# Optimization experiments

Hardware: AMD Instinct MI355X
Metric: run time of the kernel (lower is better)

The kernel has to match this reference:

```python
import jax, jax.numpy as jnp
import numpy as np

ENC_IN = 512
D_MODEL = 1024
EMB_DIM = 32
IN_DIM = D_MODEL + EMB_DIM  # 1056
BATCH = 64


def setup_inputs() -> dict:
    key = jax.random.key(0)
    ks = jax.random.split(key, 12)
    s = 0.02
    return {
        "x": jax.random.normal(ks[0], (BATCH, ENC_IN, D_MODEL), dtype=jnp.float32),
        "emb": jax.random.normal(ks[1], (ENC_IN, EMB_DIM), dtype=jnp.float32) * s,
        # weights stored [in, out] (transposed vs torch Linear, same math)
        "w1": jax.random.normal(ks[2], (IN_DIM, IN_DIM), dtype=jnp.float32) * s,
        "b1": jnp.zeros((IN_DIM,), dtype=jnp.float32),
        "wq": jax.random.normal(ks[3], (IN_DIM, IN_DIM), dtype=jnp.float32) * s,
        "bq": jnp.zeros((IN_DIM,), dtype=jnp.float32),
        "wk": jax.random.normal(ks[4], (IN_DIM, IN_DIM), dtype=jnp.float32) * s,
        "bk": jnp.zeros((IN_DIM,), dtype=jnp.float32),
        "wv": jax.random.normal(ks[5], (IN_DIM, IN_DIM), dtype=jnp.float32) * s,
        "bv": jnp.zeros((IN_DIM,), dtype=jnp.float32),
        "w2": jax.random.normal(ks[6], (IN_DIM, D_MODEL), dtype=jnp.float32) * s,
        "b2": jnp.zeros((D_MODEL,), dtype=jnp.float32),
    }


def reference(x, emb, w1, b1, wq, bq, wk, bk, wv, bv, w2, b2):
    B = x.shape[0]
    # variable embedding: same for every batch element -> broadcast concat
    e = jnp.broadcast_to(emb[None, :, :], (B, ENC_IN, EMB_DIM))
    h = jnp.concatenate([x, e], axis=2)                      # [B, S, IN_DIM]
    h = jax.nn.leaky_relu(h @ w1 + b1, negative_slope=0.2)   # l1
    # hand-rolled self-attention: no scaling, softmax over last dim
    q = h @ wq + bq
    k = h @ wk + bk
    v = h @ wv + bv
    energy = jnp.einsum("bsd,btd->bst", q, k)                # [B, S, S]
    attn = jax.nn.softmax(energy, axis=-1)
    out = jnp.einsum("bst,btd->bsd", attn, v)                # [B, S, IN_DIM]
    return out @ w2 + b2                                     # [B, S, D_MODEL]
```

## Files before the change

### kernel.cpp

```cpp
#include <hip/hip_runtime.h>
#include <hip/hip_bf16.h>
#include <cstdint>

typedef __hip_bfloat16 bf16;
typedef __attribute__((ext_vector_type(8))) short short8;
typedef __attribute__((ext_vector_type(4))) float f32x4;

__device__ __forceinline__ void gload16(const bf16* g, bf16* l) {
    __builtin_amdgcn_global_load_lds(
        (__attribute__((address_space(1))) void*)g,
        (__attribute__((address_space(3))) void*)l, 16, 0, 0);
}
#define VMC(n) asm volatile("s_waitcnt vmcnt(" #n ")" ::: "memory")
__device__ __forceinline__ void bar() {
    asm volatile("" ::: "memory");
    __builtin_amdgcn_s_barrier();
    asm volatile("" ::: "memory");
}

__device__ __forceinline__ void stage_half(const bf16* __restrict__ G, int ld,
                                           int row0, int k0, bf16* lregion,
                                           int w, int lrow, int lslot)
{
    const bf16* s0 = G + (long long)(row0 + w * 8 + lrow) * ld + (k0 + lslot * 8);
    gload16(s0, lregion + (w * 64) * 8);
    gload16(s0 + (long long)64 * ld, lregion + (512 + w * 64) * 8);
}

#define LOAD_AI(dst, i_, mh, P) do { \
    _Pragma("unroll") for (int ks_ = 0; ks_ < 2; ++ks_) \
      dst[i_][ks_] = *(const short8*)((P) + ((mh) * 64 + (i_) * 16 + l15) * 64 \
                                         + (((ks_ * 4 + lq) ^ l7) * 8)); } while (0)
#define LOAD_B(nh, dst) do { _Pragma("unroll") for (int j_ = 0; j_ < 2; ++j_) { \
    _Pragma("unroll") for (int ks_ = 0; ks_ < 2; ++ks_) \
      dst[j_][ks_] = *(const short8*)(pb + (bhr + (nh) * 32 + j_ * 16 + l15) * 64 \
                                         + (((ks_ * 4 + lq) ^ l7) * 8)); } } while (0)
#define DO_Q(mh, nh, AF, BF) do { \
    __builtin_amdgcn_s_setprio(1); \
    _Pragma("unroll") for (int i_ = 0; i_ < 4; ++i_) \
      _Pragma("unroll") for (int j_ = 0; j_ < 2; ++j_) \
        _Pragma("unroll") for (int ks_ = 0; ks_ < 2; ++ks_) \
          acc[mh][nh][i_][j_] = __builtin_amdgcn_mfma_f32_16x16x32_bf16( \
              AF[i_][ks_], BF[j_][ks_], acc[mh][nh][i_][j_], 0, 0, 0); \
    __builtin_amdgcn_s_setprio(0); \
} while (0)

template<int OUT_BF16, int ACT, int HAS_BIAS, int ROUTE>
__global__ __launch_bounds__(512, 2)
void gemm256(const bf16* __restrict__ Abase, const bf16* __restrict__ Bbase,
             void* __restrict__ Cbase, const float* __restrict__ bias,
             int K, int lda, int ldb, int ldc, int nwrite,
             long long sA, long long sB, long long sC, long long segStride)
{
    __shared__ bf16 lds[2][2][2][8192];

    const int gx = gridDim.x, gy = gridDim.y;
    const int nwg = gx * gy * gridDim.z;
    const int lin = blockIdx.x + gx * (blockIdx.y + gy * blockIdx.z);
    const int qch = nwg >> 3, rch = nwg & 7;
    const int xcd = lin & 7, pos = lin >> 3;
    const int nl = (xcd < rch ? xcd * (qch + 1)
                              : rch * (qch + 1) + (xcd - rch) * qch) + pos;
    const int bz = nl / (gx * gy);
    const int rem = nl - bz * (gx * gy);
    const int by = rem / gx;
    const int bx = rem - by * gx;

    const int tid = threadIdx.x;
    const int wid = tid >> 6, lane = tid & 63;
    const int wm = wid >> 2, wn = wid & 3;
    const int l15 = lane & 15, l7 = lane & 7, lq = lane >> 4;
    const int lrow = lane >> 3, lslot = l7 ^ lrow;
    const int bhr = (wn & 1) * 64;

    const bf16* A = Abase + (long long)bz * sA;
    const bf16* B = Bbase + (long long)bz * sB;
    const int brow = by * 256, bcol = bx * 256;

    f32x4 acc[2][2][4][2] = {};
    short8 aFe[4][2], aFo[4][2], bF0[2][2], bF1[2][2];

    const int nt = K >> 6;

    stage_half(B, ldb, bcol,       0,  &lds[0][1][0][0], wid, lrow, lslot);
    stage_half(B, ldb, bcol + 128, 0,  &lds[0][1][1][0], wid, lrow, lslot);
    stage_half(A, lda, brow,       0,  &lds[0][0][0][0], wid, lrow, lslot);
    stage_half(A, lda, brow + 128, 0,  &lds[0][0][1][0], wid, lrow, lslot);
    stage_half(B, ldb, bcol,       64, &lds[1][1][0][0], wid, lrow, lslot);
    stage_half(B, ldb, bcol + 128, 64, &lds[1][1][1][0], wid, lrow, lslot);
    VMC(4);
    bar();

    for (int t = 0; t < nt; ++t) {
        const int b = t & 1;
        const bf16* pa = &lds[b][0][wm][0];
        const bf16* pb = &lds[b][1][wn >> 1][0];
        bf16* oA = &lds[b ^ 1][0][0][0];
        bf16* cB = &lds[b][1][0][0];
        const int t1 = (t + 1 == nt) ? 0 : t + 1;
        const int t2 = (t + 2 >= nt) ? t + 2 - nt : t + 2;
        const int k1 = t1 << 6, k2 = t2 << 6;

        LOAD_B(0, bF0);
        LOAD_AI(aFe, 0, 0, pa); LOAD_AI(aFe, 1, 0, pa);
        LOAD_AI(aFe, 2, 0, pa); LOAD_AI(aFe, 3, 0, pa);
        LOAD_B(1, bF1);
        stage_half(A, lda, brow, k1, oA, wid, lrow, lslot);
        bar();
        DO_Q(0, 0, aFe, bF0);
        bar();

        LOAD_AI(aFo, 0, 1, pa); LOAD_AI(aFo, 1, 1, pa);
        stage_half(A, lda, brow + 128, k1, oA + 8192, wid, lrow, lslot);
        bar();
        DO_Q(0, 1, aFe, bF1);
        bar();

        LOAD_AI(aFo, 2, 1, pa); LOAD_AI(aFo, 3, 1, pa);
        stage_half(B, ldb, bcol, k2, cB, wid, lrow, lslot);
        bar();
        DO_Q(1, 1, aFo, bF1);
        bar();

        stage_half(B, ldb, bcol + 128, k2, cB + 8192, wid, lrow, lslot);
        bar();
        DO_Q(1, 0, aFo, bF0);
        VMC(4);
        bar();
    }
    VMC(0);

    const long long cofs0 = (long long)bz * sC;
    #pragma unroll
    for (int mh = 0; mh < 2; ++mh)
      #pragma unroll
      for (int nh = 0; nh < 2; ++nh)
        #pragma unroll
        for (int i = 0; i < 4; ++i)
          #pragma unroll
          for (int j = 0; j < 2; ++j) {
              const int gc = bcol + wn * 64 + nh * 32 + j * 16 + l15;
              int lc = gc;
              long long cofs = cofs0;
              if (ROUTE) {
                  const unsigned seg = (unsigned)gc / 1152u;
                  lc = gc - (int)(seg * 1152u);
                  cofs += (long long)seg * segStride;
              }
              const bool wr = gc < nwrite;
              const float bvv = (HAS_BIAS && wr) ? bias[gc] : 0.0f;
              const int row0 = brow + wm * 128 + mh * 64 + i * 16 + lq * 4;
              if (wr) {
                  #pragma unroll
                  for (int rr = 0; rr < 4; ++rr) {
                      float vv = acc[mh][nh][i][j][rr] + bvv;
                      if (ACT) vv = vv > 0.0f ? vv : 0.2f * vv;
                      const long long cidx = cofs + (long long)(row0 + rr) * ldc + lc;
                      if (OUT_BF16) ((bf16*)Cbase)[cidx] = (bf16)vv;
                      else          ((float*)Cbase)[cidx] = vv;
                  }
              }
          }
}

__global__ void concat_cast_kernel(const float* __restrict__ x,
                                   const float* __restrict__ emb,
                                   bf16* __restrict__ out)
{
    const int m = blockIdx.x;
    const int s = m & 511;
    const float* xr = x + (long long)m * 1024;
    bf16* orow = out + (long long)m * 1088;
    for (int g = threadIdx.x; g < 272; g += 256) {
        const int c = g * 4;
        float4 v;
        if (c < 1024)      v = *(const float4*)&xr[c];
        else if (c < 1056) v = *(const float4*)&emb[s * 32 + (c - 1024)];
        else               v = make_float4(0.f, 0.f, 0.f, 0.f);
        bf16 t[4] = { (bf16)v.x, (bf16)v.y, (bf16)v.z, (bf16)v.w };
        *(ushort4*)&orow[c] = *(ushort4*)t;
    }
}

__global__ void wtrans5_kernel(const float* __restrict__ w1, const float* __restrict__ wq,
                               const float* __restrict__ wk, const float* __restrict__ wv,
                               const float* __restrict__ w2,
                               bf16* __restrict__ w1T, bf16* __restrict__ wqkvT,
                               bf16* __restrict__ w2T)
{
    const int z = blockIdx.z;
    const float* src; bf16* dst; int NIN, NP, srcld;
    switch (z) {
        case 0: src = w1; dst = w1T;                   NIN = 1056; NP = 1280; srcld = 1056; break;
        case 1: src = wq; dst = wqkvT;                 NIN = 1056; NP = 1152; srcld = 1056; break;
        case 2: src = wk; dst = wqkvT + 1152LL * 1088; NIN = 1056; NP = 1152; srcld = 1056; break;
        case 3: src = wv; dst = wqkvT + 2304LL * 1088; NIN = 1056; NP = 1280; srcld = 1056; break;
        default: src = w2; dst = w2T;                  NIN = 1024; NP = 1024; srcld = 1024; break;
    }
    const int KIN = 1056, KP = 1088;
    const int k0 = blockIdx.x * 32, n0 = blockIdx.y * 32;
    if (n0 >= NP) return;
    __shared__ float t[32][33];
    const int tx = threadIdx.x, ty = threadIdx.y;
    const int kk = k0 + ty, nn = n0 + tx;
    t[ty][tx] = (kk < KIN && nn < NIN) ? src[(long long)kk * srcld + nn] : 0.0f;
    __syncthreads();
    const int ko = k0 + tx, no = n0 + ty;
    if (no < NP && ko < KP)
        dst[(long long)no * KP + ko] = (bf16)t[tx][ty];
}

__global__ void biasprep_kernel(const float* __restrict__ b1, const float* __restrict__ bq,
                                const float* __restrict__ bk, const float* __restrict__ bv,
                                const float* __restrict__ b2,
                                float* __restrict__ b1p, float* __restrict__ bqkv,
                                float* __restrict__ b2p)
{
    const int i = blockIdx.x * 256 + threadIdx.x;
    if (i < 1280) {
        b1p[i] = (i < 1056) ? b1[i] : 0.0f;
    } else if (i < 1280 + 3456) {
        const int j = i - 1280;
        const int seg = j / 1152, c = j - seg * 1152;
        const float* src = seg == 0 ? bq : (seg == 1 ? bk : bv);
        bqkv[j] = (c < 1056) ? src[c] : 0.0f;
    } else if (i < 1280 + 3456 + 1024) {
        b2p[i - (1280 + 3456)] = b2[i - (1280 + 3456)];
    }
}

__global__ void vtrans_kernel(const bf16* __restrict__ v, bf16* __restrict__ vt)
{
    __shared__ bf16 t[64][72];
    const long long b = blockIdx.z;
    const bf16* vb = v + b * (512LL * 1152);
    bf16* vtb = vt + b * (1280LL * 512);
    const int d0 = blockIdx.x * 64, s0 = blockIdx.y * 64;
    const int tx = threadIdx.x & 15, ty = threadIdx.x >> 4;
    const bool zz = d0 >= 1152;
    #pragma unroll
    for (int i = 0; i < 4; ++i) {
        const int row = ty + i * 16;
        ushort4 val = make_ushort4(0, 0, 0, 0);
        if (!zz)
            val = *(const ushort4*)&vb[(long long)(s0 + row) * 1152 + d0 + tx * 4];
        *(ushort4*)&t[row][tx * 4] = val;
    }
    __syncthreads();
    #pragma unroll
    for (int i = 0; i < 4; ++i) {
        const int d = ty + i * 16;
        ushort4 o;
        o.x = *(const ushort*)&t[tx * 4 + 0][d];
        o.y = *(const ushort*)&t[tx * 4 + 1][d];
        o.z = *(const ushort*)&t[tx * 4 + 2][d];
        o.w = *(const ushort*)&t[tx * 4 + 3][d];
        *(ushort4*)&vtb[(long long)(d0 + d) * 512 + s0 + tx * 4] = o;
    }
}

__global__ __launch_bounds__(256)
void softmax_kernel(const float* __restrict__ e, bf16* __restrict__ p)
{
    const int wid = threadIdx.x >> 6, lane = threadIdx.x & 63;
    const long long row = (long long)blockIdx.x * 4 + wid;
    const float* er = e + row * 512;
    float v[8];
    float mx = -3.0e38f;
    #pragma unroll
    for (int j = 0; j < 8; ++j) { v[j] = er[j * 64 + lane]; mx = fmaxf(mx, v[j]); }
    #pragma unroll
    for (int s = 32; s > 0; s >>= 1) mx = fmaxf(mx, __shfl_xor(mx, s));
    float sum = 0.0f;
    #pragma unroll
    for (int j = 0; j < 8; ++j) { v[j] = __expf(v[j] - mx); sum += v[j]; }
    #pragma unroll
    for (int s = 32; s > 0; s >>= 1) sum += __shfl_xor(sum, s);
    const float inv = 1.0f / sum;
    bf16* pr = p + row * 512;
    #pragma unroll
    for (int j = 0; j < 8; ++j) pr[j * 64 + lane] = (bf16)(v[j] * inv);
}

extern "C" void kernel_launch(void* const* d_in, const int* in_sizes, int n_in,
                              void* d_out, int out_size, void* d_ws, size_t ws_size,
                              hipStream_t stream)
{
    const float* x   = (const float*)d_in[0];
    const float* emb = (const float*)d_in[1];
    const float* w1  = (const float*)d_in[2];
    const float* b1  = (const float*)d_in[3];
    const float* wq  = (const float*)d_in[4];
    const float* bq  = (const float*)d_in[5];
    const float* wk  = (const float*)d_in[6];
    const float* bk  = (const float*)d_in[7];
    const float* wv  = (const float*)d_in[8];
    const float* bv  = (const float*)d_in[9];
    const float* w2  = (const float*)d_in[10];
    const float* b2  = (const float*)d_in[11];
    float* out = (float*)d_out;

    const long long Mrows = 32768;
    const int KR = 1088;
    const int WQ = 1152;

    char* ws = (char*)d_ws;
    size_t off = 0;
    auto alloc = [&](size_t bytes) -> char* {
        char* p = ws + off;
        off += (bytes + 255) & ~(size_t)255;
        return p;
    };
    char* R1    = alloc((size_t)Mrows * KR * 2);
    char* R2    = alloc((size_t)64 * 1280 * 512 * 2);
    bf16* qkv   = (bf16*)alloc((size_t)3 * Mrows * WQ * 2);
    bf16* w1T   = (bf16*)alloc((size_t)1280 * KR * 2);
    bf16* wqkvT = (bf16*)alloc((size_t)3584 * KR * 2);
    bf16* w2T   = (bf16*)alloc((size_t)1024 * KR * 2);
    float* b1p  = (float*)alloc((size_t)1280 * 4);
    float* bqkv = (float*)alloc((size_t)3456 * 4);
    float* b2p  = (float*)alloc((size_t)1024 * 4);

    bf16*  hcat   = (bf16*)R1;
    float* energy = (float*)R1;
    bf16*  pv     = (bf16*)R1;
    bf16*  h      = (bf16*)R2;
    bf16*  vT     = (bf16*)R2;
    bf16*  qb     = qkv;
    bf16*  kb     = qkv + Mrows * WQ;
    bf16*  vb     = qkv + 2 * Mrows * WQ;
    bf16*  attn   = kb;

    concat_cast_kernel<<<32768, 256, 0, stream>>>(x, emb, hcat);
    wtrans5_kernel<<<dim3(34, 40, 5), dim3(32, 32), 0, stream>>>(
        w1, wq, wk, wv, w2, w1T, wqkvT, w2T);
    biasprep_kernel<<<23, 256, 0, stream>>>(b1, bq, bk, bv, b2, b1p, bqkv, b2p);

    gemm256<1, 1, 1, 0><<<dim3(5, 128, 1), 512, 0, stream>>>(
        hcat, w1T, h, b1p, KR, KR, KR, KR, KR, 0, 0, 0, 0);
    gemm256<1, 0, 1, 1><<<dim3(14, 128, 1), 512, 0, stream>>>(
        h, wqkvT, qkv, bqkv, KR, KR, KR, WQ, 3456, 0, 0, 0,
        (long long)Mrows * WQ);
    vtrans_kernel<<<dim3(20, 8, 64), 256, 0, stream>>>(vb, vT);
    gemm256<0, 0, 0, 0><<<dim3(2, 2, 64), 512, 0, stream>>>(
        qb, kb, energy, nullptr, KR, WQ, WQ, 512, 512,
        512LL * WQ, 512LL * WQ, 512LL * 512, 0);
    softmax_kernel<<<8192, 256, 0, stream>>>(energy, attn);
    gemm256<1, 0, 0, 0><<<dim3(5, 2, 64), 512, 0, stream>>>(
        attn, vT, pv, nullptr, 512, 512, 512, KR, KR,
        512LL * 512, 1280LL * 512, 512LL * KR, 0);
    gemm256<0, 0, 1, 0><<<dim3(4, 128, 1), 512, 0, stream>>>(
        pv, w2T, out, b2p, KR, KR, KR, 1024, 1024, 0, 0, 0, 0);
}
```

Measured before the change: 669.2 us.

## Fold Wq·Wkᵀ into one projection to drop the K projection

Energy is rewritten as q·kᵀ = h(Wq Wkᵀ)hᵀ plus a per-row term, so only one projection (h·Wq Wkᵀ) plus V is computed instead of separate Q and K. Energy becomes a batched GEMM of that projection against h, with the bias handled by a precomputed vector u = Wk·bq and a per-row scalar c = h·u. This removes about a third of the projection GEMM and a large Q/K intermediate. In exchange it adds a small weight-product GEMM, extra prep kernels, and some rounding differences from the bf16 combined weight.

```diff
diff --git a/kernel.cpp b/kernel.cpp
--- a/kernel.cpp
+++ b/kernel.cpp
@@ -45,7 +45,7 @@
     __builtin_amdgcn_s_setprio(0); \
 } while (0)
 
-template<int OUT_BF16, int ACT, int HAS_BIAS, int ROUTE>
+template<int OUT_BF16, int ACT, int BIASMODE, int ROUTE>
 __global__ __launch_bounds__(512, 2)
 void gemm256(const bf16* __restrict__ Abase, const bf16* __restrict__ Bbase,
              void* __restrict__ Cbase, const float* __restrict__ bias,
@@ -140,22 +140,22 @@
           #pragma unroll
           for (int j = 0; j < 2; ++j) {
               const int gc = bcol + wn * 64 + nh * 32 + j * 16 + l15;
-              int lc = gc;
-              long long cofs = cofs0;
-              if (ROUTE) {
-                  const unsigned seg = (unsigned)gc / 1152u;
-                  lc = gc - (int)(seg * 1152u);
-                  cofs += (long long)seg * segStride;
-              }
               const bool wr = gc < nwrite;
-              const float bvv = (HAS_BIAS && wr) ? bias[gc] : 0.0f;
               const int row0 = brow + wm * 128 + mh * 64 + i * 16 + lq * 4;
               if (wr) {
+                  float bvv = 0.0f;
+                  if (BIASMODE == 1) bvv = bias[gc];
+                  if (BIASMODE == 3) bvv = bias[(long long)bz * 512 + gc];
+                  long long base; int lc, ld;
+                  if (ROUTE == 2) {
+                      if (gc < 1152) { base = 0; lc = gc; ld = 1152; }
+                      else { base = segStride; lc = gc - 1152; ld = 1088; }
+                  } else { base = cofs0; lc = gc; ld = ldc; }
                   #pragma unroll
                   for (int rr = 0; rr < 4; ++rr) {
                       float vv = acc[mh][nh][i][j][rr] + bvv;
                       if (ACT) vv = vv > 0.0f ? vv : 0.2f * vv;
-                      const long long cidx = cofs + (long long)(row0 + rr) * ldc + lc;
+                      const long long cidx = base + (long long)(row0 + rr) * ld + lc;
                       if (OUT_BF16) ((bf16*)Cbase)[cidx] = (bf16)vv;
                       else          ((float*)Cbase)[cidx] = vv;
                   }
@@ -182,20 +182,17 @@
     }
 }
 
-__global__ void wtrans5_kernel(const float* __restrict__ w1, const float* __restrict__ wq,
-                               const float* __restrict__ wk, const float* __restrict__ wv,
+__global__ void wtrans3_kernel(const float* __restrict__ w1, const float* __restrict__ wv,
                                const float* __restrict__ w2,
-                               bf16* __restrict__ w1T, bf16* __restrict__ wqkvT,
+                               bf16* __restrict__ w1T, bf16* __restrict__ Bqv,
                                bf16* __restrict__ w2T)
 {
     const int z = blockIdx.z;
     const float* src; bf16* dst; int NIN, NP, srcld;
     switch (z) {
-        case 0: src = w1; dst = w1T;                   NIN = 1056; NP = 1280; srcld = 1056; break;
-        case 1: src = wq; dst = wqkvT;                 NIN = 1056; NP = 1152; srcld = 1056; break;
-        case 2: src = wk; dst = wqkvT + 1152LL * 1088; NIN = 1056; NP = 1152; srcld = 1056; break;
-        case 3: src = wv; dst = wqkvT + 2304LL * 1088; NIN = 1056; NP = 1280; srcld = 1056; break;
-        default: src = w2; dst = w2T;                  NIN = 1024; NP = 1024; srcld = 1024; break;
+        case 0: src = w1; dst = w1T; NIN = 1056; NP = 1280; srcld = 1056; break;
+        case 1: src = wv; dst = Bqv; NIN = 1056; NP = 1152; srcld = 1056; break;
+        default: src = w2; dst = w2T; NIN = 1024; NP = 1024; srcld = 1024; break;
     }
     const int KIN = 1056, KP = 1088;
     const int k0 = blockIdx.x * 32, n0 = blockIdx.y * 32;
@@ -210,22 +207,63 @@
         dst[(long long)no * KP + ko] = (bf16)t[tx][ty];
 }
 
-__global__ void biasprep_kernel(const float* __restrict__ b1, const float* __restrict__ bq,
-                                const float* __restrict__ bk, const float* __restrict__ bv,
+__global__ void wcast2_kernel(const float* __restrict__ wq, const float* __restrict__ wk,
+                              bf16* __restrict__ wqC, bf16* __restrict__ wkC)
+{
+    const int i = blockIdx.x;
+    const float* src = blockIdx.y ? wk : wq;
+    bf16* dst = blockIdx.y ? wkC : wqC;
+    for (int c = threadIdx.x; c < 1088; c += 256) {
+        float v = (i < 1056 && c < 1056) ? src[(long long)i * 1056 + c] : 0.0f;
+        dst[(long long)i * 1088 + c] = (bf16)v;
+    }
+}
+
+__global__ void uvec_kernel(const float* __restrict__ wk, const float* __restrict__ bq,
+                            float* __restrict__ u)
+{
+    const int wid = threadIdx.x >> 6, lane = threadIdx.x & 63;
+    const int e = blockIdx.x * 4 + wid;
+    if (e >= 1088) return;
+    float s = 0.0f;
+    if (e < 1056) {
+        for (int d = lane; d < 1056; d += 64)
+            s += wk[(long long)e * 1056 + d] * bq[d];
+    }
+    #pragma unroll
+    for (int sh = 32; sh > 0; sh >>= 1) s += __shfl_xor(s, sh);
+    if (lane == 0) u[e] = s;
+}
+
+__global__ __launch_bounds__(256)
+void cvec_kernel(const bf16* __restrict__ h, const float* __restrict__ u,
+                 float* __restrict__ c)
+{
+    const int wid = threadIdx.x >> 6, lane = threadIdx.x & 63;
+    const long long row = (long long)blockIdx.x * 4 + wid;
+    const bf16* hr = h + row * 1088;
+    float s = 0.0f;
+    #pragma unroll
+    for (int j = 0; j < 17; ++j)
+        s += (float)hr[j * 64 + lane] * u[j * 64 + lane];
+    #pragma unroll
+    for (int sh = 32; sh > 0; sh >>= 1) s += __shfl_xor(s, sh);
+    if (lane == 0) c[row] = s;
+}
+
+__global__ void biasprep_kernel(const float* __restrict__ b1, const float* __restrict__ bv,
                                 const float* __restrict__ b2,
-                                float* __restrict__ b1p, float* __restrict__ bqkv,
+                                float* __restrict__ b1p, float* __restrict__ bqv2,
                                 float* __restrict__ b2p)
 {
     const int i = blockIdx.x * 256 + threadIdx.x;
-    if (i < 1280) {
+    if (i < 1088) {
         b1p[i] = (i < 1056) ? b1[i] : 0.0f;
-    } else if (i < 1280 + 3456) {
-        const int j = i - 1280;
-        const int seg = j / 1152, c = j - seg * 1152;
-        const float* src = seg == 0 ? bq : (seg == 1 ? bk : bv);
-        bqkv[j] = (c < 1056) ? src[c] : 0.0f;
-    } else if (i < 1280 + 3456 + 1024) {
-        b2p[i - (1280 + 3456)] = b2[i - (1280 + 3456)];
+    } else if (i < 1088 + 2304) {
+        const int j = i - 1088;
+        bqv2[j] = (j < 1056) ? bv[j] : 0.0f;
+    } else if (i < 1088 + 2304 + 1024) {
+        b2p[i - (1088 + 2304)] = b2[i - (1088 + 2304)];
     }
 }
 
@@ -293,7 +331,6 @@
     const float* wq  = (const float*)d_in[4];
     const float* bq  = (const float*)d_in[5];
     const float* wk  = (const float*)d_in[6];
-    const float* bk  = (const float*)d_in[7];
     const float* wv  = (const float*)d_in[8];
     const float* bv  = (const float*)d_in[9];
     const float* w2  = (const float*)d_in[10];
@@ -302,7 +339,6 @@
 
     const long long Mrows = 32768;
     const int KR = 1088;
-    const int WQ = 1152;
 
     char* ws = (char*)d_ws;
     size_t off = 0;
@@ -311,40 +347,48 @@
         off += (bytes + 255) & ~(size_t)255;
         return p;
     };
-    char* R1    = alloc((size_t)Mrows * KR * 2);
-    char* R2    = alloc((size_t)64 * 1280 * 512 * 2);
-    bf16* qkv   = (bf16*)alloc((size_t)3 * Mrows * WQ * 2);
-    bf16* w1T   = (bf16*)alloc((size_t)1280 * KR * 2);
-    bf16* wqkvT = (bf16*)alloc((size_t)3584 * KR * 2);
-    bf16* w2T   = (bf16*)alloc((size_t)1024 * KR * 2);
-    float* b1p  = (float*)alloc((size_t)1280 * 4);
-    float* bqkv = (float*)alloc((size_t)3456 * 4);
+    char* R1   = alloc((size_t)Mrows * KR * 2);
+    char* Rh   = alloc((size_t)Mrows * KR * 2);
+    char* Rq   = alloc((size_t)Mrows * KR * 2);
+    bf16* vbuf = (bf16*)alloc((size_t)Mrows * 1152 * 2);
+    bf16* vT   = (bf16*)alloc((size_t)64 * 1280 * 512 * 2);
+    bf16* w1T  = (bf16*)alloc((size_t)1280 * KR * 2);
+    bf16* Bqv  = (bf16*)alloc((size_t)2432 * KR * 2);
+    bf16* w2T  = (bf16*)alloc((size_t)1024 * KR * 2);
+    bf16* wqC  = (bf16*)alloc((size_t)1280 * KR * 2);
+    bf16* wkC  = (bf16*)alloc((size_t)1280 * KR * 2);
+    float* b1p  = (float*)alloc((size_t)1088 * 4);
+    float* bqv2 = (float*)alloc((size_t)2304 * 4);
     float* b2p  = (float*)alloc((size_t)1024 * 4);
+    float* uvec = (float*)alloc((size_t)1088 * 4);
+    float* cvec = (float*)alloc((size_t)Mrows * 4);
 
     bf16*  hcat   = (bf16*)R1;
     float* energy = (float*)R1;
     bf16*  pv     = (bf16*)R1;
-    bf16*  h      = (bf16*)R2;
-    bf16*  vT     = (bf16*)R2;
-    bf16*  qb     = qkv;
-    bf16*  kb     = qkv + Mrows * WQ;
-    bf16*  vb     = qkv + 2 * Mrows * WQ;
-    bf16*  attn   = kb;
+    bf16*  h      = (bf16*)Rh;
+    bf16*  qbuf   = (bf16*)Rq;
+    bf16*  attn   = (bf16*)Rq;
 
     concat_cast_kernel<<<32768, 256, 0, stream>>>(x, emb, hcat);
-    wtrans5_kernel<<<dim3(34, 40, 5), dim3(32, 32), 0, stream>>>(
-        w1, wq, wk, wv, w2, w1T, wqkvT, w2T);
-    biasprep_kernel<<<23, 256, 0, stream>>>(b1, bq, bk, bv, b2, b1p, bqkv, b2p);
-
+    wtrans3_kernel<<<dim3(34, 40, 3), dim3(32, 32), 0, stream>>>(
+        w1, wv, w2, w1T, Bqv, w2T);
+    wcast2_kernel<<<dim3(1280, 2), 256, 0, stream>>>(wq, wk, wqC, wkC);
+    uvec_kernel<<<272, 256, 0, stream>>>(wk, bq, uvec);
+    biasprep_kernel<<<18, 256, 0, stream>>>(b1, bv, b2, b1p, bqv2, b2p);
+
+    gemm256<1, 0, 0, 0><<<dim3(5, 5, 1), 512, 0, stream>>>(
+        wkC, wqC, Bqv + 1152LL * KR, nullptr, KR, KR, KR, KR, KR, 0, 0, 0, 0);
     gemm256<1, 1, 1, 0><<<dim3(5, 128, 1), 512, 0, stream>>>(
         hcat, w1T, h, b1p, KR, KR, KR, KR, KR, 0, 0, 0, 0);
-    gemm256<1, 0, 1, 1><<<dim3(14, 128, 1), 512, 0, stream>>>(
-        h, wqkvT, qkv, bqkv, KR, KR, KR, WQ, 3456, 0, 0, 0,
-        (long long)Mrows * WQ);
-    vtrans_kernel<<<dim3(20, 8, 64), 256, 0, stream>>>(vb, vT);
-    gemm256<0, 0, 0, 0><<<dim3(2, 2, 64), 512, 0, stream>>>(
-        qb, kb, energy, nullptr, KR, WQ, WQ, 512, 512,
-        512LL * WQ, 512LL * WQ, 512LL * 512, 0);
+    cvec_kernel<<<8192, 256, 0, stream>>>(h, uvec, cvec);
+    gemm256<1, 0, 1, 2><<<dim3(9, 128, 1), 512, 0, stream>>>(
+        h, Bqv, vbuf, bqv2, KR, KR, KR, 0, 2240, 0, 0, 0,
+        (long long)(qbuf - vbuf));
+    vtrans_kernel<<<dim3(20, 8, 64), 256, 0, stream>>>(vbuf, vT);
+    gemm256<0, 0, 3, 0><<<dim3(2, 2, 64), 512, 0, stream>>>(
+        qbuf, h, energy, cvec, KR, KR, KR, 512, 512,
+        512LL * KR, 512LL * KR, 512LL * 512, 0);
     softmax_kernel<<<8192, 256, 0, stream>>>(energy, attn);
     gemm256<1, 0, 0, 0><<<dim3(5, 2, 64), 512, 0, stream>>>(
         attn, vT, pv, nullptr, 512, 512, 512, KR, KR,
```

Measured after the change: 633.5 us. -5.3%, faster.
